# Performance work log

Hardware: AMD Instinct MI355X
Metric: run time of the kernel (lower is better)

## Reference

```python
import jax, jax.numpy as jnp
import numpy as np

B, N_MAX, D_MODEL, K_F, ROD_ID_DIM = 16384, 64, 256, 8, 8
BETA = 10000.0
PRECOMP = 64  # FourierFeatures precompute_limit
DISK_FEAT = 2 + 2 * K_F + 3 + ROD_ID_DIM   # 29
ROD_FEAT = 2 + 1 + 1 + 2 * 2 * K_F + ROD_ID_DIM  # 44


def fourier_table():
    # sin/cos interleaved as in torch: stack([sin,cos],-1).view(P, 2K)
    k = jnp.arange(K_F, dtype=jnp.float32)
    omega = BETA ** (-2.0 * k / (2.0 * K_F))
    idx = jnp.arange(PRECOMP, dtype=jnp.float32)
    oi = idx[:, None] * omega  # (P, K)
    return jnp.stack([jnp.sin(oi), jnp.cos(oi)], axis=-1).reshape(PRECOMP, 2 * K_F)


def setup_inputs() -> dict:
    key = jax.random.key(0)
    ks = jax.random.split(key, 8)
    state = jax.random.randint(ks[0], (B, N_MAX), 0, 3, dtype=jnp.int32)
    s = 0.02
    return {
        'state': state,
        'rod_id_embed': jax.random.normal(ks[1], (3, ROD_ID_DIM), jnp.float32),
        'disk_W': jax.random.normal(ks[2], (DISK_FEAT, D_MODEL), jnp.float32) * s,
        'disk_b': jax.random.normal(ks[3], (D_MODEL,), jnp.float32) * s,
        'rod_W': jax.random.normal(ks[4], (ROD_FEAT, D_MODEL), jnp.float32) * s,
        'rod_b': jax.random.normal(ks[5], (D_MODEL,), jnp.float32) * s,
        'null_fourier': jax.random.normal(ks[6], (2 * K_F,), jnp.float32) * s,
        'padding_embedding': jax.random.normal(ks[7], (D_MODEL,), jnp.float32) * s,
    }


def reference(state, rod_id_embed, disk_W, disk_b, rod_W, rod_b, null_fourier, padding_embedding):
    Bq, N = state.shape
    table = fourier_table()                      # (P, 2K)
    valid = state != -1                          # (B, N)
    lengths = valid.sum(axis=1)                  # (B,)
    state_safe = jnp.clip(state, 0, 2)

    # ---- vectorized _compute_state_info ----
    onehot = (state[:, None, :] == jnp.arange(3, dtype=state.dtype)[None, :, None]) & valid[:, None, :]  # (B,3,N)
    oh = onehot.astype(jnp.float32)
    counts = oh.sum(-1)                          # (B,3) disks per rod
    is_empty = counts == 0.0
    len_norm = counts / jnp.maximum(lengths, 1).astype(jnp.float32)[:, None]
    top_disk = jnp.argmax(onehot, axis=-1)       # min index on rod (top = smallest disk)
    bottom_disk = (N - 1) - jnp.argmax(onehot[:, :, ::-1], axis=-1)
    # per-disk: 'above' = # of smaller-index disks on same rod (exclusive prefix sum)
    cum = jnp.cumsum(oh, axis=-1) - oh           # (B,3,N)
    above = jnp.take_along_axis(cum, state_safe[:, None, :], axis=1)[:, 0, :]   # (B,N)
    height = jnp.take_along_axis(counts, state_safe, axis=1)                    # (B,N)
    vf = valid.astype(jnp.float32)
    is_top = (above == 0.0).astype(jnp.float32) * vf
    is_bottom = (above == height - 1.0).astype(jnp.float32) * vf
    depth_norm = jnp.where(height > 1.0, above / jnp.maximum(height - 1.0, 1.0), 0.0) * vf

    # ---- rod nodes (3) ----
    rod_type = jnp.broadcast_to(jnp.array([0.0, 1.0], jnp.float32), (Bq, 3, 2))
    top_f = table[top_disk]                      # (B,3,2K)
    bot_f = table[bottom_disk]
    emp = is_empty[:, :, None]
    top_f = jnp.where(emp, null_fourier, top_f)
    bot_f = jnp.where(emp, null_fourier, bot_f)
    rod_ids = jnp.broadcast_to(rod_id_embed[None], (Bq, 3, ROD_ID_DIM))
    rod_feats = jnp.concatenate([
        rod_type, len_norm[:, :, None], emp.astype(jnp.float32), top_f, bot_f, rod_ids], axis=-1)  # (B,3,44)
    rod_emb = jnp.einsum('brf,fd->brd', rod_feats, rod_W) + rod_b

    # ---- disk nodes (N) ----
    disk_type = jnp.broadcast_to(jnp.array([1.0, 0.0], jnp.float32), (Bq, N, 2))
    size_f = jnp.broadcast_to(table[:N][None], (Bq, N, 2 * K_F))
    rod_id_vec = rod_id_embed[state_safe]        # (B,N,rod_id_dim)
    disk_feats = jnp.concatenate([
        disk_type, size_f, depth_norm[:, :, None], is_top[:, :, None], is_bottom[:, :, None], rod_id_vec], axis=-1)  # (B,N,29)
    disk_emb = jnp.einsum('bnf,fd->bnd', disk_feats, disk_W) + disk_b
    disk_emb = jnp.where(valid[:, :, None], disk_emb, padding_embedding)

    return jnp.concatenate([rod_emb, disk_emb], axis=1)  # (B, 3+N, d_model)
```

## Files before the change

kernel.cpp:

```cpp
#include <hip/hip_runtime.h>

#define DM 256
#define NMAX 64

#define OFF_RIDPROJ 16384
#define OFF_BASEROD 17152
#define OFF_RODTOP  17920
#define OFF_RODBOT  34560

typedef float vf4 __attribute__((ext_vector_type(4)));

static __device__ __forceinline__ vf4 ld4(const float* p) {
  return *reinterpret_cast<const vf4*>(p);
}
static __device__ __forceinline__ void st4_nt(float* p, vf4 v) {
  __builtin_nontemporal_store(v, reinterpret_cast<vf4*>(p));
}

__global__ void precomp_kernel(
    const float* __restrict__ rod_id_embed,
    const float* __restrict__ disk_W,
    const float* __restrict__ disk_b,
    const float* __restrict__ rod_W,
    const float* __restrict__ rod_b,
    const float* __restrict__ null_fourier,
    float* __restrict__ ws) {
  const int idx = blockIdx.x;
  const int d = threadIdx.x;

  float F[16];
  if (idx < 64) {
#pragma unroll
    for (int k = 0; k < 8; ++k) {
      float omega = powf(10000.0f, -(float)k * 0.125f);
      float a = (float)idx * omega;
      F[2 * k]     = sinf(a);
      F[2 * k + 1] = cosf(a);
    }
  } else {
#pragma unroll
    for (int k = 0; k < 16; ++k) F[k] = null_fourier[k];
  }

  float* baseDisk = ws;
  float* ridproj  = ws + OFF_RIDPROJ;
  float* baseRod  = ws + OFF_BASEROD;
  float* rodTop   = ws + OFF_RODTOP;
  float* rodBot   = ws + OFF_RODBOT;

  float t = 0.f, bo = 0.f;
#pragma unroll
  for (int k = 0; k < 16; ++k) {
    t  += F[k] * rod_W[(4 + k) * DM + d];
    bo += F[k] * rod_W[(20 + k) * DM + d];
  }
  rodTop[idx * DM + d] = t;
  rodBot[idx * DM + d] = bo;

  if (idx < 64) {
    float base = disk_b[d] + disk_W[0 * DM + d];
#pragma unroll
    for (int k = 0; k < 16; ++k) base += F[k] * disk_W[(2 + k) * DM + d];
    baseDisk[(size_t)idx * DM + d] = base;
  }
  if (idx < 3) {
    float rp = 0.f;
    float br = rod_b[d] + rod_W[1 * DM + d];
#pragma unroll
    for (int j = 0; j < 8; ++j) {
      rp += rod_id_embed[idx * 8 + j] * disk_W[(21 + j) * DM + d];
      br += rod_id_embed[idx * 8 + j] * rod_W[(36 + j) * DM + d];
    }
    ridproj[idx * DM + d] = rp;
    baseRod[idx * DM + d] = br;
  }
}

#define BLK_B 8

__launch_bounds__(512)
__global__ void enc_kernel(
    const int* __restrict__ state,
    const float* __restrict__ disk_W,
    const float* __restrict__ rod_W,
    const float* __restrict__ padding_embedding,
    const float* __restrict__ ws,
    float* __restrict__ out,
    int Btot) {
  const float* baseDisk = ws;
  const float* ridproj  = ws + OFF_RIDPROJ;
  const float* baseRod  = ws + OFF_BASEROD;
  const float* rodTop   = ws + OFF_RODTOP;
  const float* rodBot   = ws + OFF_RODBOT;

  const int tid  = threadIdx.x;
  const int w    = tid >> 6;
  const int lane = tid & 63;
  long b = (long)blockIdx.x * BLK_B + w;
  if (b >= Btot) b = Btot - 1;

  __shared__ float base_sh[64 * DM];
  __shared__ vf4  meta_sh[BLK_B][64];
  __shared__ float lnorm_sh[BLK_B][3];
  __shared__ float emp_sh[BLK_B][3];
  __shared__ int   ti_sh[BLK_B][3];
  __shared__ int   bi_sh[BLK_B][3];

#pragma unroll
  for (int k = 0; k < 8; ++k) {
    const int i4 = tid + k * 512;
    *(reinterpret_cast<vf4*>(base_sh) + i4) = ld4(baseDisk + (size_t)i4 * 4);
  }

  const int s = state[b * NMAX + lane];
  const bool valid = (s >= 0);
  const int ss = s <= 0 ? 0 : (s >= 2 ? 2 : s);
  const unsigned long long m0 = __ballot(valid && s == 0);
  const unsigned long long m1 = __ballot(valid && s == 1);
  const unsigned long long m2 = __ballot(valid && s == 2);
  const unsigned long long vm = __ballot(valid);
  const unsigned long long mym = (ss == 0) ? m0 : ((ss == 1) ? m1 : m2);
  const int above  = __popcll(mym & ((1ull << lane) - 1ull));
  const int height = __popcll(mym);

  vf4 md;
  md.x = valid ? (float)(ss + 1) : 0.f;
  md.y = (valid && height > 1) ? (float)above / (float)(height - 1) : 0.f;
  md.z = (valid && above == 0) ? 1.f : 0.f;
  md.w = (valid && above == height - 1) ? 1.f : 0.f;
  meta_sh[w][lane] = md;

  if (lane < 3) {
    const unsigned long long m = (lane == 0) ? m0 : ((lane == 1) ? m1 : m2);
    const int cnt = __popcll(m);
    const int lengths = __popcll(vm);
    lnorm_sh[w][lane] = (float)cnt / (float)(lengths > 1 ? lengths : 1);
    emp_sh[w][lane]   = (cnt == 0) ? 1.f : 0.f;
    ti_sh[w][lane]    = cnt ? (int)__builtin_ctzll(m) : 64;
    bi_sh[w][lane]    = cnt ? 63 - (int)__builtin_clzll(m) : 64;
  }
  __syncthreads();

  const int c0 = lane * 4;
  const vf4 Wdep = ld4(disk_W + 18 * DM + c0);
  const vf4 Wt   = ld4(disk_W + 19 * DM + c0);
  const vf4 Wb   = ld4(disk_W + 20 * DM + c0);
  const vf4 pad  = ld4(padding_embedding + c0);
  const vf4 rW2  = ld4(rod_W + 2 * DM + c0);
  const vf4 rW3  = ld4(rod_W + 3 * DM + c0);
  const vf4 rp0  = ld4(ridproj + 0 * DM + c0);
  const vf4 rp1  = ld4(ridproj + 1 * DM + c0);
  const vf4 rp2  = ld4(ridproj + 2 * DM + c0);

  float* outB = out + (size_t)b * 67 * DM;

#pragma unroll
  for (int r = 0; r < 3; ++r) {
    const float ln = lnorm_sh[w][r];
    const float em = emp_sh[w][r];
    const int ti = ti_sh[w][r];
    const int bi = bi_sh[w][r];
    vf4 v = ld4(baseRod + r * DM + c0);
    const vf4 tf = ld4(rodTop + (size_t)ti * DM + c0);
    const vf4 bf = ld4(rodBot + (size_t)bi * DM + c0);
    v += ln * rW2 + em * rW3 + tf + bf;
    st4_nt(outB + r * DM + c0, v);
  }

#pragma unroll 8
  for (int i = 0; i < 64; ++i) {
    const vf4 md2 = meta_sh[w][i];
    vf4 v;
    if (md2.x > 0.5f) {
      const vf4 base = ld4(base_sh + i * DM + c0);
      const vf4 rp = (md2.x < 1.5f) ? rp0 : ((md2.x < 2.5f) ? rp1 : rp2);
      v = base + rp + md2.y * Wdep + md2.z * Wt + md2.w * Wb;
    } else {
      v = pad;
    }
    st4_nt(outB + (size_t)(3 + i) * DM + c0, v);
  }
}

extern "C" void kernel_launch(void* const* d_in, const int* in_sizes, int n_in,
                              void* d_out, int out_size, void* d_ws, size_t ws_size,
                              hipStream_t stream) {
  const int*   state             = (const int*)d_in[0];
  const float* rod_id_embed      = (const float*)d_in[1];
  const float* disk_W            = (const float*)d_in[2];
  const float* disk_b            = (const float*)d_in[3];
  const float* rod_W             = (const float*)d_in[4];
  const float* rod_b             = (const float*)d_in[5];
  const float* null_fourier      = (const float*)d_in[6];
  const float* padding_embedding = (const float*)d_in[7];
  float* ws  = (float*)d_ws;
  float* out = (float*)d_out;

  const int B = in_sizes[0] / NMAX;

  hipLaunchKernelGGL(precomp_kernel, dim3(65), dim3(256), 0, stream,
                     rod_id_embed, disk_W, disk_b, rod_W, rod_b, null_fourier, ws);
  hipLaunchKernelGGL(enc_kernel, dim3((B + BLK_B - 1) / BLK_B), dim3(512), 0, stream,
                     state, disk_W, rod_W, padding_embedding, ws, out, B);
}
```

Baseline: 223.4 us.

## Use one block per batch row with readlane broadcast instead of LDS staging

Each 256-thread block now handles one batch row, with four wavefronts splitting the 67 output rows instead of one wavefront writing all rows for its batch element. The 64 KB LDS copy of the disk base table and the shared metadata arrays are removed. Per-disk flags and depth are broadcast with readlane, and the base table is read from global or L2 memory. This drops the large per-block LDS fill and the barrier and raises occupancy, at the cost of many more blocks and repeated per-block state processing.

```diff
diff --git a/kernel.cpp b/kernel.cpp
--- a/kernel.cpp
+++ b/kernel.cpp
@@ -76,17 +76,14 @@
   }
 }
 
-#define BLK_B 8
-
-__launch_bounds__(512)
+__launch_bounds__(256)
 __global__ void enc_kernel(
     const int* __restrict__ state,
     const float* __restrict__ disk_W,
     const float* __restrict__ rod_W,
     const float* __restrict__ padding_embedding,
     const float* __restrict__ ws,
-    float* __restrict__ out,
-    int Btot) {
+    float* __restrict__ out) {
   const float* baseDisk = ws;
   const float* ridproj  = ws + OFF_RIDPROJ;
   const float* baseRod  = ws + OFF_BASEROD;
@@ -94,23 +91,9 @@
   const float* rodBot   = ws + OFF_RODBOT;
 
   const int tid  = threadIdx.x;
-  const int w    = tid >> 6;
+  const int q    = tid >> 6;
   const int lane = tid & 63;
-  long b = (long)blockIdx.x * BLK_B + w;
-  if (b >= Btot) b = Btot - 1;
-
-  __shared__ float base_sh[64 * DM];
-  __shared__ vf4  meta_sh[BLK_B][64];
-  __shared__ float lnorm_sh[BLK_B][3];
-  __shared__ float emp_sh[BLK_B][3];
-  __shared__ int   ti_sh[BLK_B][3];
-  __shared__ int   bi_sh[BLK_B][3];
-
-#pragma unroll
-  for (int k = 0; k < 8; ++k) {
-    const int i4 = tid + k * 512;
-    *(reinterpret_cast<vf4*>(base_sh) + i4) = ld4(baseDisk + (size_t)i4 * 4);
-  }
+  const long b   = blockIdx.x;
 
   const int s = state[b * NMAX + lane];
   const bool valid = (s >= 0);
@@ -123,62 +106,83 @@
   const int above  = __popcll(mym & ((1ull << lane) - 1ull));
   const int height = __popcll(mym);
 
-  vf4 md;
-  md.x = valid ? (float)(ss + 1) : 0.f;
-  md.y = (valid && height > 1) ? (float)above / (float)(height - 1) : 0.f;
-  md.z = (valid && above == 0) ? 1.f : 0.f;
-  md.w = (valid && above == height - 1) ? 1.f : 0.f;
-  meta_sh[w][lane] = md;
-
-  if (lane < 3) {
-    const unsigned long long m = (lane == 0) ? m0 : ((lane == 1) ? m1 : m2);
-    const int cnt = __popcll(m);
-    const int lengths = __popcll(vm);
-    lnorm_sh[w][lane] = (float)cnt / (float)(lengths > 1 ? lengths : 1);
-    emp_sh[w][lane]   = (cnt == 0) ? 1.f : 0.f;
-    ti_sh[w][lane]    = cnt ? (int)__builtin_ctzll(m) : 64;
-    bi_sh[w][lane]    = cnt ? 63 - (int)__builtin_clzll(m) : 64;
-  }
-  __syncthreads();
+  const float depf = (valid && height > 1) ? (float)above / (float)(height - 1) : 0.f;
+  const int flags = valid ? ((ss + 1) | (above == 0 ? 4 : 0) |
+                             (above == height - 1 ? 8 : 0))
+                          : 0;
+
+  const unsigned long long mr = (lane == 0) ? m0 : ((lane == 1) ? m1 : m2);
+  const int cnt = __popcll(mr);
+  const int lengths = __popcll(vm);
+  const float lnf = (float)cnt / (float)(lengths > 1 ? lengths : 1);
+  const int ti = cnt ? (int)__builtin_ctzll(mr) : 64;
+  const int bi = cnt ? 63 - (int)__builtin_clzll(mr) : 64;
+  const int rodpack = ti | (bi << 8) | ((cnt == 0) ? 0x10000 : 0);
 
   const int c0 = lane * 4;
   const vf4 Wdep = ld4(disk_W + 18 * DM + c0);
   const vf4 Wt   = ld4(disk_W + 19 * DM + c0);
   const vf4 Wb   = ld4(disk_W + 20 * DM + c0);
   const vf4 pad  = ld4(padding_embedding + c0);
-  const vf4 rW2  = ld4(rod_W + 2 * DM + c0);
-  const vf4 rW3  = ld4(rod_W + 3 * DM + c0);
   const vf4 rp0  = ld4(ridproj + 0 * DM + c0);
   const vf4 rp1  = ld4(ridproj + 1 * DM + c0);
   const vf4 rp2  = ld4(ridproj + 2 * DM + c0);
 
   float* outB = out + (size_t)b * 67 * DM;
 
-#pragma unroll
-  for (int r = 0; r < 3; ++r) {
-    const float ln = lnorm_sh[w][r];
-    const float em = emp_sh[w][r];
-    const int ti = ti_sh[w][r];
-    const int bi = bi_sh[w][r];
-    vf4 v = ld4(baseRod + r * DM + c0);
-    const vf4 tf = ld4(rodTop + (size_t)ti * DM + c0);
-    const vf4 bf = ld4(rodBot + (size_t)bi * DM + c0);
-    v += ln * rW2 + em * rW3 + tf + bf;
-    st4_nt(outB + r * DM + c0, v);
-  }
-
-#pragma unroll 8
-  for (int i = 0; i < 64; ++i) {
-    const vf4 md2 = meta_sh[w][i];
+  if (q < 3) {
+    const vf4 rW2 = ld4(rod_W + 2 * DM + c0);
+    const vf4 rW3 = ld4(rod_W + 3 * DM + c0);
+    const float ln = __uint_as_float(
+        __builtin_amdgcn_readlane(__float_as_uint(lnf), q));
+    const int rpk = __builtin_amdgcn_readlane(rodpack, q);
+    const int rti = rpk & 0xff;
+    const int rbi = (rpk >> 8) & 0xff;
+    const float em = (float)((rpk >> 16) & 1);
+    vf4 v = ld4(baseRod + q * DM + c0);
+    v += ld4(rodTop + (size_t)rti * DM + c0);
+    v += ld4(rodBot + (size_t)rbi * DM + c0);
+    v += ln * rW2 + em * rW3;
+    st4_nt(outB + q * DM + c0, v);
+  }
+
+#pragma unroll 4
+  for (int r = q + 4; r < 67; r += 4) {
+    const int i = r - 3;
+    const int fl = __builtin_amdgcn_readlane(flags, i);
+    const float dep = __uint_as_float(
+        __builtin_amdgcn_readlane(__float_as_uint(depf), i));
     vf4 v;
-    if (md2.x > 0.5f) {
-      const vf4 base = ld4(base_sh + i * DM + c0);
-      const vf4 rp = (md2.x < 1.5f) ? rp0 : ((md2.x < 2.5f) ? rp1 : rp2);
-      v = base + rp + md2.y * Wdep + md2.z * Wt + md2.w * Wb;
+    if (fl) {
+      const vf4 base = ld4(baseDisk + (size_t)i * DM + c0);
+      const int code = fl & 3;
+      const vf4 rp = (code == 1) ? rp0 : ((code == 2) ? rp1 : rp2);
+      const float tt = (float)((fl >> 2) & 1);
+      const float bb = (float)((fl >> 3) & 1);
+      v = base + rp + dep * Wdep + tt * Wt + bb * Wb;
     } else {
       v = pad;
     }
-    st4_nt(outB + (size_t)(3 + i) * DM + c0, v);
+    st4_nt(outB + (size_t)r * DM + c0, v);
+  }
+
+  if (q == 3) {
+    const int i = 0;
+    const int fl = __builtin_amdgcn_readlane(flags, i);
+    const float dep = __uint_as_float(
+        __builtin_amdgcn_readlane(__float_as_uint(depf), i));
+    vf4 v;
+    if (fl) {
+      const vf4 base = ld4(baseDisk + (size_t)i * DM + c0);
+      const int code = fl & 3;
+      const vf4 rp = (code == 1) ? rp0 : ((code == 2) ? rp1 : rp2);
+      const float tt = (float)((fl >> 2) & 1);
+      const float bb = (float)((fl >> 3) & 1);
+      v = base + rp + dep * Wdep + tt * Wt + bb * Wb;
+    } else {
+      v = pad;
+    }
+    st4_nt(outB + 3 * DM + c0, v);
   }
 }
 
@@ -200,6 +204,6 @@
 
   hipLaunchKernelGGL(precomp_kernel, dim3(65), dim3(256), 0, stream,
                      rod_id_embed, disk_W, disk_b, rod_W, rod_b, null_fourier, ws);
-  hipLaunchKernelGGL(enc_kernel, dim3((B + BLK_B - 1) / BLK_B), dim3(512), 0, stream,
-                     state, disk_W, rod_W, padding_embedding, ws, out, B);
-}
+  hipLaunchKernelGGL(enc_kernel, dim3(B), dim3(256), 0, stream,
+                     state, disk_W, rod_W, padding_embedding, ws, out);
+}
```

Result: no change. 223.6 us (+0.1%).
